# Kernel tuning notes

Measured on AMD Instinct MI355X. Metric: run time of the kernel, lower is better.

The kernel has to match this reference:

```python
import jax, jax.numpy as jnp
import numpy as np

N_NODES = 50000
N_EDGES = 600000
F_IN = 128
H_DIM = 256
N_CLASSES = 16
N_GRAPHS = 64


def _sage_conv(x, edge_index, W_l, W_r, b, num_nodes):
    # PyG SAGEConv (aggr='mean', root_weight=True):
    #   out = lin_l(mean_{j in N(i)} x_j) + lin_r(x_i)
    src, dst = edge_index[0], edge_index[1]
    msg_sum = jax.ops.segment_sum(x[src], dst, num_segments=num_nodes)      # [N, F]
    cnt = jax.ops.segment_sum(jnp.ones((edge_index.shape[1],), x.dtype), dst,
                              num_segments=num_nodes)                        # [N]
    mean = msg_sum / jnp.maximum(cnt, 1.0)[:, None]
    return mean @ W_l + x @ W_r + b


def _global_mean_pool(x, batch, num_graphs):
    s = jax.ops.segment_sum(x, batch, num_segments=num_graphs)               # [G, C]
    c = jax.ops.segment_sum(jnp.ones((x.shape[0],), x.dtype), batch,
                            num_segments=num_graphs)                         # [G]
    return s / jnp.maximum(c, 1.0)[:, None]


def setup_inputs() -> dict:
    key = jax.random.key(0)
    ks = jax.random.split(key, 9)
    x = jax.random.normal(ks[0], (N_NODES, F_IN), dtype=jnp.float32)
    edge_index = jax.random.randint(ks[1], (2, N_EDGES), 0, N_NODES)
    batch = jnp.sort(jax.random.randint(ks[2], (N_NODES,), 0, N_GRAPHS))
    # SAGEConv params (glorot-ish scale)
    def w(k, fi, fo):
        return jax.random.normal(k, (fi, fo), dtype=jnp.float32) / np.sqrt(fi)
    return {
        "x": x,
        "edge_index": edge_index,
        "batch": batch,
        "W1_l": w(ks[3], F_IN, H_DIM),
        "W1_r": w(ks[4], F_IN, H_DIM),
        "b1": jnp.zeros((H_DIM,), jnp.float32),
        "W2_l": w(ks[5], H_DIM, N_CLASSES),
        "W2_r": w(ks[6], H_DIM, N_CLASSES),
        "b2": jnp.zeros((N_CLASSES,), jnp.float32),
    }


def reference(x, edge_index, batch, W1_l, W1_r, b1, W2_l, W2_r, b2):
    n = x.shape[0]
    h = _sage_conv(x, edge_index, W1_l, W1_r, b1, n)
    h = jax.nn.relu(h)
    h = _sage_conv(h, edge_index, W2_l, W2_r, b2, n)
    h = jax.nn.relu(h)
    g = _global_mean_pool(h, batch, N_GRAPHS)
    return jax.nn.log_softmax(g, axis=1)
```

## Files before the change

### kernel.cpp

```cpp
#include <hip/hip_runtime.h>

#define N_NODES   50000
#define N_EDGES   600000
#define F_IN      128
#define H_DIM     256
#define N_CLASSES 16
#define N_GRAPHS  64
#define M_PAD     50048
#define MAX_DEG   64
#define ZERO_WORDS (50000 + 1024 + 64 + 1)

typedef unsigned short ushort_t;
typedef unsigned int   uint_t;
typedef __attribute__((ext_vector_type(8))) short bf16x8;
typedef __attribute__((ext_vector_type(4))) float f32x4;

__device__ inline ushort_t f2bf(float f) {
    union { float f; uint_t u; } v; v.f = f;
    uint_t r = v.u + 0x7FFF + ((v.u >> 16) & 1);
    return (ushort_t)(r >> 16);
}
__device__ inline float bf2f(uint_t u) {
    union { uint_t u; float f; } v; v.u = u << 16;
    return v.f;
}
__device__ inline void load_lds16(const void* g, void* l) {
    __builtin_amdgcn_global_load_lds(
        (const __attribute__((address_space(1))) void*)g,
        (__attribute__((address_space(3))) void*)l, 16, 0, 0);
}

__global__ __launch_bounds__(256) void prep_kernel(
    const float* __restrict__ x,
    const float* __restrict__ W1l, const float* __restrict__ W1r,
    const float* __restrict__ W2l, const float* __restrict__ W2r,
    uint_t* __restrict__ wszero, ushort_t* __restrict__ ha,
    ushort_t* __restrict__ Bt, ushort_t* __restrict__ Bt2) {
    const int t = blockIdx.x * blockDim.x + threadIdx.x;
    if (t < ZERO_WORDS) wszero[t] = 0u;
    if (t < 65536) {
        const int n = t >> 8, k = t & 255;
        const float v = (k < 128) ? W1l[k * H_DIM + n] : W1r[(k - 128) * H_DIM + n];
        Bt[n * 256 + k] = f2bf(v);
    } else if (t < 65536 + 8192) {
        const int t2 = t - 65536;
        const int c = t2 >> 8, k = t2 & 255;
        const float v = (c < 16) ? W2l[k * N_CLASSES + c] : W2r[k * N_CLASSES + (c - 16)];
        Bt2[c * 256 + k] = f2bf(v);
    }
    if (t >= N_NODES * 32) return;
    const int n = t >> 5, c = t & 31;
    const float4 v = *reinterpret_cast<const float4*>(x + (size_t)n * F_IN + c * 4);
    uint2 pk;
    pk.x = (uint_t)f2bf(v.x) | ((uint_t)f2bf(v.y) << 16);
    pk.y = (uint_t)f2bf(v.z) | ((uint_t)f2bf(v.w) << 16);
    *reinterpret_cast<uint2*>(ha + (size_t)n * 256 + 128 + c * 4) = pk;
}

__global__ void scatter_pad_kernel(const int* __restrict__ src,
                                   const int* __restrict__ dst,
                                   int* __restrict__ cnt,
                                   int* __restrict__ slots) {
    int e = blockIdx.x * blockDim.x + threadIdx.x;
    if (e >= N_EDGES) return;
    const int d = dst[e];
    const int pos = atomicAdd(&cnt[d], 1);
    if (pos < MAX_DEG) slots[d * MAX_DEG + pos] = src[e];
}

__global__ __launch_bounds__(256) void agg1_kernel(const int* __restrict__ cnt,
                                                   const int* __restrict__ slots,
                                                   ushort_t* __restrict__ ha,
                                                   float* __restrict__ invdeg) {
    const int n = blockIdx.x * 4 + (threadIdx.x >> 6);
    if (n >= N_NODES) return;
    const int lane = threadIdx.x & 63;
    const int slot = lane >> 3;
    const int c    = lane & 7;
    const int deg  = min(cnt[n], MAX_DEG);
    const int* srow = slots + n * MAX_DEG;
    float a[16];
#pragma unroll
    for (int i = 0; i < 16; ++i) a[i] = 0.f;
    for (int e = slot; e < deg; e += 16) {
        const int s0 = srow[e];
        const ushort_t* r0 = ha + (size_t)s0 * 256 + 128;
        const uint4 v00 = *reinterpret_cast<const uint4*>(r0 + c * 8);
        const uint4 v01 = *reinterpret_cast<const uint4*>(r0 + 64 + c * 8);
        const int e1 = e + 8;
        uint4 v10, v11;
        if (e1 < deg) {
            const int s1 = srow[e1];
            const ushort_t* r1 = ha + (size_t)s1 * 256 + 128;
            v10 = *reinterpret_cast<const uint4*>(r1 + c * 8);
            v11 = *reinterpret_cast<const uint4*>(r1 + 64 + c * 8);
        }
        a[0] += bf2f(v00.x & 0xFFFFu); a[1] += bf2f(v00.x >> 16);
        a[2] += bf2f(v00.y & 0xFFFFu); a[3] += bf2f(v00.y >> 16);
        a[4] += bf2f(v00.z & 0xFFFFu); a[5] += bf2f(v00.z >> 16);
        a[6] += bf2f(v00.w & 0xFFFFu); a[7] += bf2f(v00.w >> 16);
        a[8]  += bf2f(v01.x & 0xFFFFu); a[9]  += bf2f(v01.x >> 16);
        a[10] += bf2f(v01.y & 0xFFFFu); a[11] += bf2f(v01.y >> 16);
        a[12] += bf2f(v01.z & 0xFFFFu); a[13] += bf2f(v01.z >> 16);
        a[14] += bf2f(v01.w & 0xFFFFu); a[15] += bf2f(v01.w >> 16);
        if (e1 < deg) {
            a[0] += bf2f(v10.x & 0xFFFFu); a[1] += bf2f(v10.x >> 16);
            a[2] += bf2f(v10.y & 0xFFFFu); a[3] += bf2f(v10.y >> 16);
            a[4] += bf2f(v10.z & 0xFFFFu); a[5] += bf2f(v10.z >> 16);
            a[6] += bf2f(v10.w & 0xFFFFu); a[7] += bf2f(v10.w >> 16);
            a[8]  += bf2f(v11.x & 0xFFFFu); a[9]  += bf2f(v11.x >> 16);
            a[10] += bf2f(v11.y & 0xFFFFu); a[11] += bf2f(v11.y >> 16);
            a[12] += bf2f(v11.z & 0xFFFFu); a[13] += bf2f(v11.z >> 16);
            a[14] += bf2f(v11.w & 0xFFFFu); a[15] += bf2f(v11.w >> 16);
        }
    }
#pragma unroll
    for (int i = 0; i < 16; ++i) {
        a[i] += __shfl_xor(a[i], 8);
        a[i] += __shfl_xor(a[i], 16);
        a[i] += __shfl_xor(a[i], 32);
    }
    const float iv = 1.0f / fmaxf((float)deg, 1.0f);
    if (slot == 0) {
        uint4 pk0, pk1;
        pk0.x = (uint_t)f2bf(a[0] * iv) | ((uint_t)f2bf(a[1] * iv) << 16);
        pk0.y = (uint_t)f2bf(a[2] * iv) | ((uint_t)f2bf(a[3] * iv) << 16);
        pk0.z = (uint_t)f2bf(a[4] * iv) | ((uint_t)f2bf(a[5] * iv) << 16);
        pk0.w = (uint_t)f2bf(a[6] * iv) | ((uint_t)f2bf(a[7] * iv) << 16);
        pk1.x = (uint_t)f2bf(a[8]  * iv) | ((uint_t)f2bf(a[9]  * iv) << 16);
        pk1.y = (uint_t)f2bf(a[10] * iv) | ((uint_t)f2bf(a[11] * iv) << 16);
        pk1.z = (uint_t)f2bf(a[12] * iv) | ((uint_t)f2bf(a[13] * iv) << 16);
        pk1.w = (uint_t)f2bf(a[14] * iv) | ((uint_t)f2bf(a[15] * iv) << 16);
        ushort_t* orow = ha + (size_t)n * 256;
        *reinterpret_cast<uint4*>(orow + c * 8) = pk0;
        *reinterpret_cast<uint4*>(orow + 64 + c * 8) = pk1;
        if (c == 0) invdeg[n] = iv;
    }
}

__global__ __launch_bounds__(256) void gemm1_fused_kernel(
    const ushort_t* __restrict__ ha, const ushort_t* __restrict__ Bt,
    const ushort_t* __restrict__ Bt2, const float* __restrict__ b1,
    float* __restrict__ p, float* __restrict__ r) {
    __shared__ ushort_t sA[64 * 256];
    __shared__ ushort_t sB[32 * 256];
    const int tid  = threadIdx.x;
    const int mblk = blockIdx.x;

    const char* gA = (const char*)ha + (size_t)mblk * 32768;
    const char* gB = (const char*)Bt;
#pragma unroll
    for (int i = 0; i < 8; ++i) {
        const int d = (i * 256 + tid) * 16;
        const int s = d ^ (((d >> 9) & 7) << 4);
        load_lds16(gA + s, (char*)sA + (d & ~1023));
    }
#pragma unroll
    for (int i = 0; i < 4; ++i) {
        const int d = (i * 256 + tid) * 16;
        const int s = d ^ (((d >> 9) & 7) << 4);
        load_lds16(gB + s, (char*)sB + (d & ~1023));
    }
    __syncthreads();

    const int w    = tid >> 6;
    const int lane = tid & 63;
    const int lr   = lane & 15;
    const int hi   = lane >> 4;
    const int m0   = w * 16;

    bf16x8 afr[8];
    {
        const int row = m0 + lr;
        const int sw = (row & 7) << 4;
#pragma unroll
        for (int ks = 0; ks < 8; ++ks)
            afr[ks] = *reinterpret_cast<const bf16x8*>(
                (const char*)sA + ((row * 512 + ks * 64 + hi * 16) ^ sw));
    }

    f32x4 acc[16];
#pragma unroll
    for (int t = 0; t < 16; ++t) acc[t] = (f32x4){0.f, 0.f, 0.f, 0.f};

#pragma unroll
    for (int ph = 0; ph < 8; ++ph) {
#pragma unroll
        for (int fnl = 0; fnl < 2; ++fnl) {
            const int rn = fnl * 16 + lr;
            const int sw = (rn & 7) << 4;
#pragma unroll
            for (int ks = 0; ks < 8; ++ks) {
                const bf16x8 bfr = *reinterpret_cast<const bf16x8*>(
                    (const char*)sB + ((rn * 512 + ks * 64 + hi * 16) ^ sw));
                acc[ph * 2 + fnl] = __builtin_amdgcn_mfma_f32_16x16x32_bf16(
                    afr[ks], bfr, acc[ph * 2 + fnl], 0, 0, 0);
            }
        }
        __syncthreads();
        if (ph < 7) {
#pragma unroll
            for (int i = 0; i < 4; ++i) {
                const int d = (i * 256 + tid) * 16;
                const int s = d ^ (((d >> 9) & 7) << 4);
                load_lds16(gB + (ph + 1) * 16384 + s, (char*)sB + (d & ~1023));
            }
            __syncthreads();
        }
    }

#pragma unroll
    for (int t = 0; t < 16; ++t) {
        const int colG = t * 16 + lr;
        const float bias = b1[colG];
#pragma unroll
        for (int i = 0; i < 4; ++i) {
            const int row = m0 + hi * 4 + i;
            const float h = fmaxf(acc[t][i] + bias, 0.f);
            const int ad = (row * 512 + colG * 2) ^ ((row & 7) << 4);
            *reinterpret_cast<ushort_t*>((char*)sA + ad) = f2bf(h);
        }
    }
    __syncthreads();

    const char* bt2b = (const char*)Bt2;
    const int nr = m0 + lr;
    const int swn = (nr & 7) << 4;
    f32x4 acc2[2] = {(f32x4){0.f, 0.f, 0.f, 0.f}, (f32x4){0.f, 0.f, 0.f, 0.f}};
#pragma unroll
    for (int fc = 0; fc < 2; ++fc) {
#pragma unroll
        for (int k2 = 0; k2 < 8; ++k2) {
            const bf16x8 a2 = *reinterpret_cast<const bf16x8*>(
                bt2b + (fc * 16 + lr) * 512 + k2 * 64 + hi * 16);
            const bf16x8 b2 = *reinterpret_cast<const bf16x8*>(
                (const char*)sA + ((nr * 512 + k2 * 64 + hi * 16) ^ swn));
            acc2[fc] = __builtin_amdgcn_mfma_f32_16x16x32_bf16(a2, b2, acc2[fc], 0, 0, 0);
        }
    }

    const int node = mblk * 64 + nr;
    if (node < N_NODES) {
#pragma unroll
        for (int i = 0; i < 4; ++i) {
            p[(size_t)node * N_CLASSES + hi * 4 + i] = acc2[0][i];
            r[(size_t)node * N_CLASSES + hi * 4 + i] = acc2[1][i];
        }
    }
}

__global__ __launch_bounds__(256) void agg2_kernel(const float* __restrict__ p,
                                                   const int* __restrict__ cnt,
                                                   const int* __restrict__ slots,
                                                   float* __restrict__ psum) {
    const int n = blockIdx.x * 4 + (threadIdx.x >> 6);
    if (n >= N_NODES) return;
    const int lane = threadIdx.x & 63;
    const int slot = lane >> 2;
    const int c    = lane & 3;
    const int deg  = min(cnt[n], MAX_DEG);
    const int* srow = slots + n * MAX_DEG;
    float4 acc = {0.f, 0.f, 0.f, 0.f};
    for (int e = slot; e < deg; e += 16) {
        const int s = srow[e];
        const float4 v = *reinterpret_cast<const float4*>(p + (size_t)s * N_CLASSES + c * 4);
        acc.x += v.x; acc.y += v.y; acc.z += v.z; acc.w += v.w;
    }
#pragma unroll
    for (int o = 4; o < 64; o <<= 1) {
        acc.x += __shfl_xor(acc.x, o);
        acc.y += __shfl_xor(acc.y, o);
        acc.z += __shfl_xor(acc.z, o);
        acc.w += __shfl_xor(acc.w, o);
    }
    if (slot == 0)
        *reinterpret_cast<float4*>(psum + (size_t)n * N_CLASSES + c * 4) = acc;
}

__global__ __launch_bounds__(256) void pool_lsm_kernel(
    const float* __restrict__ psum, const float* __restrict__ r,
    const float* __restrict__ invdeg, const float* __restrict__ b2,
    const int* __restrict__ batch,
    float* __restrict__ gsum, float* __restrict__ gcnt,
    int* __restrict__ done, float* __restrict__ out, int nblocks) {
    __shared__ float lgsum[N_GRAPHS * N_CLASSES];
    __shared__ float lgcnt[N_GRAPHS];
    __shared__ int gminmax[2];
    __shared__ int last;
    const int t = threadIdx.x;
    const int base = blockIdx.x * 64;
#pragma unroll
    for (int k = 0; k < 4; ++k) lgsum[t + 256 * k] = 0.f;
    if (t < N_GRAPHS) lgcnt[t] = 0.f;
    if (t == 0) {
        gminmax[0] = batch[base];
        int lastn = base + 63; if (lastn >= N_NODES) lastn = N_NODES - 1;
        gminmax[1] = batch[lastn];
    }
    __syncthreads();

    const int j = t & 15;
    const float bj = b2[j];
#pragma unroll
    for (int k = 0; k < 4; ++k) {
        const int i = base + (t >> 4) + 16 * k;
        if (i < N_NODES) {
            float h = psum[(size_t)i * N_CLASSES + j] * invdeg[i]
                      + r[(size_t)i * N_CLASSES + j] + bj;
            h = fmaxf(h, 0.f);
            const int g = batch[i];
            atomicAdd(&lgsum[g * N_CLASSES + j], h);
            if (j == 0) atomicAdd(&lgcnt[g], 1.0f);
        }
    }
    __syncthreads();

    const int gmin = gminmax[0], gmax = gminmax[1];
    for (int gg = gmin + (t >> 4); gg <= gmax; gg += 16) {
        const float v = lgsum[gg * N_CLASSES + j];
        if (v != 0.f) atomicAdd(&gsum[gg * N_CLASSES + j], v);
    }
    if (t < N_GRAPHS) {
        const int gg = gmin + t;
        if (gg <= gmax) {
            const float c = lgcnt[gg];
            if (c != 0.f) atomicAdd(&gcnt[gg], c);
        }
    }
    __syncthreads();

    if (t == 0) {
        __threadfence();
        const int old = __hip_atomic_fetch_add(done, 1, __ATOMIC_ACQ_REL,
                                               __HIP_MEMORY_SCOPE_AGENT);
        last = (old == nblocks - 1) ? 1 : 0;
    }
    __syncthreads();

    if (last && t < N_GRAPHS) {
        const int g = t;
        const float cg = __hip_atomic_load(&gcnt[g], __ATOMIC_RELAXED,
                                           __HIP_MEMORY_SCOPE_AGENT);
        const float iv = 1.0f / fmaxf(cg, 1.0f);
        float v[N_CLASSES];
        float m = -1e30f;
#pragma unroll
        for (int jj = 0; jj < N_CLASSES; ++jj) {
            v[jj] = __hip_atomic_load(&gsum[g * N_CLASSES + jj], __ATOMIC_RELAXED,
                                      __HIP_MEMORY_SCOPE_AGENT) * iv;
            m = fmaxf(m, v[jj]);
        }
        float s = 0.f;
#pragma unroll
        for (int jj = 0; jj < N_CLASSES; ++jj) s += expf(v[jj] - m);
        const float lse = logf(s);
#pragma unroll
        for (int jj = 0; jj < N_CLASSES; ++jj)
            out[g * N_CLASSES + jj] = v[jj] - m - lse;
    }
}

extern "C" void kernel_launch(void* const* d_in, const int* in_sizes, int n_in,
                              void* d_out, int out_size, void* d_ws, size_t ws_size,
                              hipStream_t stream) {
    const float* x    = (const float*)d_in[0];
    const int*   ei   = (const int*)d_in[1];
    const int*   batch= (const int*)d_in[2];
    const float* W1l  = (const float*)d_in[3];
    const float* W1r  = (const float*)d_in[4];
    const float* b1   = (const float*)d_in[5];
    const float* W2l  = (const float*)d_in[6];
    const float* W2r  = (const float*)d_in[7];
    const float* b2   = (const float*)d_in[8];
    float* out = (float*)d_out;

    const int* src = ei;
    const int* dst = ei + N_EDGES;

    float* ws     = (float*)d_ws;
    int*   cnt    = (int*)ws;
    float* gsum   = ws + 50000;
    float* gcnt   = gsum + 1024;
    int*   done   = (int*)(gcnt + 64);
    float* invdeg = (float*)(done + 1);
    int*   slots  = (int*)(invdeg + 50000);
    ushort_t* Bt  = (ushort_t*)(slots + 3200000 + 3);
    ushort_t* Bt2 = Bt + 65536;
    ushort_t* ha  = Bt2 + 8192;
    float* p      = (float*)(ha + (size_t)M_PAD * 256);
    float* r      = p + 800000;
    float* psum   = (float*)ha;

    const int PB = 782;
    prep_kernel<<<(N_NODES * 32 + 255) / 256, 256, 0, stream>>>(
        x, W1l, W1r, W2l, W2r, (uint_t*)ws, ha, Bt, Bt2);
    scatter_pad_kernel<<<(N_EDGES + 255) / 256, 256, 0, stream>>>(src, dst, cnt, slots);
    agg1_kernel<<<(N_NODES + 3) / 4, 256, 0, stream>>>(cnt, slots, ha, invdeg);
    gemm1_fused_kernel<<<M_PAD / 64, 256, 0, stream>>>(ha, Bt, Bt2, b1, p, r);
    agg2_kernel<<<(N_NODES + 3) / 4, 256, 0, stream>>>(p, cnt, slots, psum);
    pool_lsm_kernel<<<PB, 256, 0, stream>>>(psum, r, invdeg, b2, batch,
                                            gsum, gcnt, done, out, PB);
}
```

Measured before the change: 150.6 us.

## Double-buffer weight tiles in GEMM1 and store layer-2 messages as bf16

The GEMM1 kernel now double-buffers the B-matrix tile in LDS, issuing the next phase's load before the current MFMA loop and dropping one barrier per phase. The layer-2 projected messages p are written as bf16 instead of fp32 with vectorized stores, and agg2 gathers 16-byte bf16 rows with 32 edge slots per wave. This halves the bytes moved in the random-gather aggregation and overlaps weight loads with compute. The cost is extra LDS per block and bf16 rounding of the layer-2 messages before summation.

```diff
diff --git a/kernel.cpp b/kernel.cpp
--- a/kernel.cpp
+++ b/kernel.cpp
@@ -141,9 +141,9 @@
 __global__ __launch_bounds__(256) void gemm1_fused_kernel(
     const ushort_t* __restrict__ ha, const ushort_t* __restrict__ Bt,
     const ushort_t* __restrict__ Bt2, const float* __restrict__ b1,
-    float* __restrict__ p, float* __restrict__ r) {
+    ushort_t* __restrict__ pb, float* __restrict__ r) {
     __shared__ ushort_t sA[64 * 256];
-    __shared__ ushort_t sB[32 * 256];
+    __shared__ ushort_t sB[2][32 * 256];
     const int tid  = threadIdx.x;
     const int mblk = blockIdx.x;
 
@@ -159,7 +159,7 @@
     for (int i = 0; i < 4; ++i) {
         const int d = (i * 256 + tid) * 16;
         const int s = d ^ (((d >> 9) & 7) << 4);
-        load_lds16(gB + s, (char*)sB + (d & ~1023));
+        load_lds16(gB + s, (char*)sB[0] + (d & ~1023));
     }
     __syncthreads();
 
@@ -185,6 +185,16 @@
 
 #pragma unroll
     for (int ph = 0; ph < 8; ++ph) {
+        if (ph < 7) {
+#pragma unroll
+            for (int i = 0; i < 4; ++i) {
+                const int d = (i * 256 + tid) * 16;
+                const int s = d ^ (((d >> 9) & 7) << 4);
+                load_lds16(gB + (ph + 1) * 16384 + s,
+                           (char*)sB[(ph + 1) & 1] + (d & ~1023));
+            }
+        }
+        const char* sbp = (const char*)sB[ph & 1];
 #pragma unroll
         for (int fnl = 0; fnl < 2; ++fnl) {
             const int rn = fnl * 16 + lr;
@@ -192,21 +202,12 @@
 #pragma unroll
             for (int ks = 0; ks < 8; ++ks) {
                 const bf16x8 bfr = *reinterpret_cast<const bf16x8*>(
-                    (const char*)sB + ((rn * 512 + ks * 64 + hi * 16) ^ sw));
+                    sbp + ((rn * 512 + ks * 64 + hi * 16) ^ sw));
                 acc[ph * 2 + fnl] = __builtin_amdgcn_mfma_f32_16x16x32_bf16(
                     afr[ks], bfr, acc[ph * 2 + fnl], 0, 0, 0);
             }
         }
         __syncthreads();
-        if (ph < 7) {
-#pragma unroll
-            for (int i = 0; i < 4; ++i) {
-                const int d = (i * 256 + tid) * 16;
-                const int s = d ^ (((d >> 9) & 7) << 4);
-                load_lds16(gB + (ph + 1) * 16384 + s, (char*)sB + (d & ~1023));
-            }
-            __syncthreads();
-        }
     }
 
 #pragma unroll
@@ -241,40 +242,50 @@
 
     const int node = mblk * 64 + nr;
     if (node < N_NODES) {
-#pragma unroll
-        for (int i = 0; i < 4; ++i) {
-            p[(size_t)node * N_CLASSES + hi * 4 + i] = acc2[0][i];
-            r[(size_t)node * N_CLASSES + hi * 4 + i] = acc2[1][i];
-        }
-    }
-}
-
-__global__ __launch_bounds__(256) void agg2_kernel(const float* __restrict__ p,
+        uint2 pp;
+        pp.x = (uint_t)f2bf(acc2[0][0]) | ((uint_t)f2bf(acc2[0][1]) << 16);
+        pp.y = (uint_t)f2bf(acc2[0][2]) | ((uint_t)f2bf(acc2[0][3]) << 16);
+        *reinterpret_cast<uint2*>(pb + (size_t)node * N_CLASSES + hi * 4) = pp;
+        float4 rv = {acc2[1][0], acc2[1][1], acc2[1][2], acc2[1][3]};
+        *reinterpret_cast<float4*>(r + (size_t)node * N_CLASSES + hi * 4) = rv;
+    }
+}
+
+__global__ __launch_bounds__(256) void agg2_kernel(const ushort_t* __restrict__ pb,
                                                    const int* __restrict__ cnt,
                                                    const int* __restrict__ slots,
                                                    float* __restrict__ psum) {
     const int n = blockIdx.x * 4 + (threadIdx.x >> 6);
     if (n >= N_NODES) return;
     const int lane = threadIdx.x & 63;
-    const int slot = lane >> 2;
-    const int c    = lane & 3;
+    const int slot = lane >> 1;
+    const int c    = lane & 1;
     const int deg  = min(cnt[n], MAX_DEG);
     const int* srow = slots + n * MAX_DEG;
-    float4 acc = {0.f, 0.f, 0.f, 0.f};
-    for (int e = slot; e < deg; e += 16) {
+    float a[8];
+#pragma unroll
+    for (int i = 0; i < 8; ++i) a[i] = 0.f;
+    for (int e = slot; e < deg; e += 32) {
         const int s = srow[e];
-        const float4 v = *reinterpret_cast<const float4*>(p + (size_t)s * N_CLASSES + c * 4);
-        acc.x += v.x; acc.y += v.y; acc.z += v.z; acc.w += v.w;
-    }
-#pragma unroll
-    for (int o = 4; o < 64; o <<= 1) {
-        acc.x += __shfl_xor(acc.x, o);
-        acc.y += __shfl_xor(acc.y, o);
-        acc.z += __shfl_xor(acc.z, o);
-        acc.w += __shfl_xor(acc.w, o);
-    }
-    if (slot == 0)
-        *reinterpret_cast<float4*>(psum + (size_t)n * N_CLASSES + c * 4) = acc;
+        const uint4 v = *reinterpret_cast<const uint4*>(pb + (size_t)s * N_CLASSES + c * 8);
+        a[0] += bf2f(v.x & 0xFFFFu); a[1] += bf2f(v.x >> 16);
+        a[2] += bf2f(v.y & 0xFFFFu); a[3] += bf2f(v.y >> 16);
+        a[4] += bf2f(v.z & 0xFFFFu); a[5] += bf2f(v.z >> 16);
+        a[6] += bf2f(v.w & 0xFFFFu); a[7] += bf2f(v.w >> 16);
+    }
+#pragma unroll
+    for (int i = 0; i < 8; ++i) {
+        a[i] += __shfl_xor(a[i], 2);
+        a[i] += __shfl_xor(a[i], 4);
+        a[i] += __shfl_xor(a[i], 8);
+        a[i] += __shfl_xor(a[i], 16);
+        a[i] += __shfl_xor(a[i], 32);
+    }
+    if (slot == 0) {
+        float* orow = psum + (size_t)n * N_CLASSES + c * 8;
+        *reinterpret_cast<float4*>(orow)     = (float4){a[0], a[1], a[2], a[3]};
+        *reinterpret_cast<float4*>(orow + 4) = (float4){a[4], a[5], a[6], a[7]};
+    }
 }
 
 __global__ __launch_bounds__(256) void pool_lsm_kernel(
@@ -387,8 +398,8 @@
     ushort_t* Bt  = (ushort_t*)(slots + 3200000 + 3);
     ushort_t* Bt2 = Bt + 65536;
     ushort_t* ha  = Bt2 + 8192;
-    float* p      = (float*)(ha + (size_t)M_PAD * 256);
-    float* r      = p + 800000;
+    ushort_t* pb  = ha + (size_t)M_PAD * 256;
+    float* r      = (float*)(pb + (size_t)M_PAD * 16);
     float* psum   = (float*)ha;
 
     const int PB = 782;
@@ -396,8 +407,8 @@
         x, W1l, W1r, W2l, W2r, (uint_t*)ws, ha, Bt, Bt2);
     scatter_pad_kernel<<<(N_EDGES + 255) / 256, 256, 0, stream>>>(src, dst, cnt, slots);
     agg1_kernel<<<(N_NODES + 3) / 4, 256, 0, stream>>>(cnt, slots, ha, invdeg);
-    gemm1_fused_kernel<<<M_PAD / 64, 256, 0, stream>>>(ha, Bt, Bt2, b1, p, r);
-    agg2_kernel<<<(N_NODES + 3) / 4, 256, 0, stream>>>(p, cnt, slots, psum);
+    gemm1_fused_kernel<<<M_PAD / 64, 256, 0, stream>>>(ha, Bt, Bt2, b1, pb, r);
+    agg2_kernel<<<(N_NODES + 3) / 4, 256, 0, stream>>>(pb, cnt, slots, psum);
     pool_lsm_kernel<<<PB, 256, 0, stream>>>(psum, r, invdeg, b2, batch,
                                             gsum, gcnt, done, out, PB);
 }
```

Result: slower. 159.5 us (+5.9%).

## Fuse layer-2 aggregation into pooling kernel and store projected features as bf16

Applied to the files above, without the earlier changes.

Removes the separate agg2 kernel and performs the neighbor gather-sum of layer-2 projected features inside the pooling kernel, which now handles 16 nodes per block. The projected p values are written as bf16 to halve the bytes gathered per edge, and the r/p stores become vectorized. This saves one launch and the psum write/read round trip, but gives up some accuracy in the layer-2 messages and means more blocks do shared-memory atomics and global flushes.

```diff
diff --git a/kernel.cpp b/kernel.cpp
--- a/kernel.cpp
+++ b/kernel.cpp
@@ -9,6 +9,7 @@
 #define M_PAD     50048
 #define MAX_DEG   64
 #define ZERO_WORDS (50000 + 1024 + 64 + 1)
+#define POOL_BLOCKS (M_PAD / 16)
 
 typedef unsigned short ushort_t;
 typedef unsigned int   uint_t;
@@ -141,7 +142,7 @@
 __global__ __launch_bounds__(256) void gemm1_fused_kernel(
     const ushort_t* __restrict__ ha, const ushort_t* __restrict__ Bt,
     const ushort_t* __restrict__ Bt2, const float* __restrict__ b1,
-    float* __restrict__ p, float* __restrict__ r) {
+    ushort_t* __restrict__ pb, float* __restrict__ r) {
     __shared__ ushort_t sA[64 * 256];
     __shared__ ushort_t sB[32 * 256];
     const int tid  = threadIdx.x;
@@ -241,46 +242,20 @@
 
     const int node = mblk * 64 + nr;
     if (node < N_NODES) {
-#pragma unroll
-        for (int i = 0; i < 4; ++i) {
-            p[(size_t)node * N_CLASSES + hi * 4 + i] = acc2[0][i];
-            r[(size_t)node * N_CLASSES + hi * 4 + i] = acc2[1][i];
-        }
-    }
-}
-
-__global__ __launch_bounds__(256) void agg2_kernel(const float* __restrict__ p,
-                                                   const int* __restrict__ cnt,
-                                                   const int* __restrict__ slots,
-                                                   float* __restrict__ psum) {
-    const int n = blockIdx.x * 4 + (threadIdx.x >> 6);
-    if (n >= N_NODES) return;
-    const int lane = threadIdx.x & 63;
-    const int slot = lane >> 2;
-    const int c    = lane & 3;
-    const int deg  = min(cnt[n], MAX_DEG);
-    const int* srow = slots + n * MAX_DEG;
-    float4 acc = {0.f, 0.f, 0.f, 0.f};
-    for (int e = slot; e < deg; e += 16) {
-        const int s = srow[e];
-        const float4 v = *reinterpret_cast<const float4*>(p + (size_t)s * N_CLASSES + c * 4);
-        acc.x += v.x; acc.y += v.y; acc.z += v.z; acc.w += v.w;
-    }
-#pragma unroll
-    for (int o = 4; o < 64; o <<= 1) {
-        acc.x += __shfl_xor(acc.x, o);
-        acc.y += __shfl_xor(acc.y, o);
-        acc.z += __shfl_xor(acc.z, o);
-        acc.w += __shfl_xor(acc.w, o);
-    }
-    if (slot == 0)
-        *reinterpret_cast<float4*>(psum + (size_t)n * N_CLASSES + c * 4) = acc;
+        uint2 pp;
+        pp.x = (uint_t)f2bf(acc2[0][0]) | ((uint_t)f2bf(acc2[0][1]) << 16);
+        pp.y = (uint_t)f2bf(acc2[0][2]) | ((uint_t)f2bf(acc2[0][3]) << 16);
+        *reinterpret_cast<uint2*>(pb + (size_t)node * N_CLASSES + hi * 4) = pp;
+        float4 rv = {acc2[1][0], acc2[1][1], acc2[1][2], acc2[1][3]};
+        *reinterpret_cast<float4*>(r + (size_t)node * N_CLASSES + hi * 4) = rv;
+    }
 }
 
 __global__ __launch_bounds__(256) void pool_lsm_kernel(
-    const float* __restrict__ psum, const float* __restrict__ r,
+    const ushort_t* __restrict__ pb, const float* __restrict__ r,
     const float* __restrict__ invdeg, const float* __restrict__ b2,
     const int* __restrict__ batch,
+    const int* __restrict__ cnt, const int* __restrict__ slots,
     float* __restrict__ gsum, float* __restrict__ gcnt,
     int* __restrict__ done, float* __restrict__ out, int nblocks) {
     __shared__ float lgsum[N_GRAPHS * N_CLASSES];
@@ -288,34 +263,62 @@
     __shared__ int gminmax[2];
     __shared__ int last;
     const int t = threadIdx.x;
-    const int base = blockIdx.x * 64;
+    const int base = blockIdx.x * 16;
 #pragma unroll
     for (int k = 0; k < 4; ++k) lgsum[t + 256 * k] = 0.f;
     if (t < N_GRAPHS) lgcnt[t] = 0.f;
     if (t == 0) {
-        gminmax[0] = batch[base];
-        int lastn = base + 63; if (lastn >= N_NODES) lastn = N_NODES - 1;
-        gminmax[1] = batch[lastn];
-    }
-    __syncthreads();
-
+        gminmax[0] = batch[min(base, N_NODES - 1)];
+        gminmax[1] = batch[min(base + 15, N_NODES - 1)];
+    }
+    __syncthreads();
+
+    const int w    = t >> 6;
+    const int lane = t & 63;
+    const int slot = lane >> 2;
+    const int c    = lane & 3;
+#pragma unroll
+    for (int i = 0; i < 4; ++i) {
+        const int n = base + w * 4 + i;
+        if (n >= N_NODES) break;
+        const int deg = min(cnt[n], MAX_DEG);
+        const int* srow = slots + n * MAX_DEG;
+        float a0 = 0.f, a1 = 0.f, a2 = 0.f, a3 = 0.f;
+        for (int e = slot; e < deg; e += 16) {
+            const int s = srow[e];
+            const uint2 v = *reinterpret_cast<const uint2*>(
+                pb + (size_t)s * N_CLASSES + c * 4);
+            a0 += bf2f(v.x & 0xFFFFu); a1 += bf2f(v.x >> 16);
+            a2 += bf2f(v.y & 0xFFFFu); a3 += bf2f(v.y >> 16);
+        }
+#pragma unroll
+        for (int o = 4; o < 64; o <<= 1) {
+            a0 += __shfl_xor(a0, o);
+            a1 += __shfl_xor(a1, o);
+            a2 += __shfl_xor(a2, o);
+            a3 += __shfl_xor(a3, o);
+        }
+        if (slot == 0) {
+            const float iv = invdeg[n];
+            const float4 rv = *reinterpret_cast<const float4*>(
+                r + (size_t)n * N_CLASSES + c * 4);
+            const float4 bv = *reinterpret_cast<const float4*>(b2 + c * 4);
+            const float h0 = fmaxf(a0 * iv + rv.x + bv.x, 0.f);
+            const float h1 = fmaxf(a1 * iv + rv.y + bv.y, 0.f);
+            const float h2 = fmaxf(a2 * iv + rv.z + bv.z, 0.f);
+            const float h3 = fmaxf(a3 * iv + rv.w + bv.w, 0.f);
+            const int g = batch[n];
+            atomicAdd(&lgsum[g * N_CLASSES + c * 4 + 0], h0);
+            atomicAdd(&lgsum[g * N_CLASSES + c * 4 + 1], h1);
+            atomicAdd(&lgsum[g * N_CLASSES + c * 4 + 2], h2);
+            atomicAdd(&lgsum[g * N_CLASSES + c * 4 + 3], h3);
+            if (c == 0) atomicAdd(&lgcnt[g], 1.0f);
+        }
+    }
+    __syncthreads();
+
+    const int gmin = gminmax[0], gmax = gminmax[1];
     const int j = t & 15;
-    const float bj = b2[j];
-#pragma unroll
-    for (int k = 0; k < 4; ++k) {
-        const int i = base + (t >> 4) + 16 * k;
-        if (i < N_NODES) {
-            float h = psum[(size_t)i * N_CLASSES + j] * invdeg[i]
-                      + r[(size_t)i * N_CLASSES + j] + bj;
-            h = fmaxf(h, 0.f);
-            const int g = batch[i];
-            atomicAdd(&lgsum[g * N_CLASSES + j], h);
-            if (j == 0) atomicAdd(&lgcnt[g], 1.0f);
-        }
-    }
-    __syncthreads();
-
-    const int gmin = gminmax[0], gmax = gminmax[1];
     for (int gg = gmin + (t >> 4); gg <= gmax; gg += 16) {
         const float v = lgsum[gg * N_CLASSES + j];
         if (v != 0.f) atomicAdd(&gsum[gg * N_CLASSES + j], v);
@@ -323,8 +326,8 @@
     if (t < N_GRAPHS) {
         const int gg = gmin + t;
         if (gg <= gmax) {
-            const float c = lgcnt[gg];
-            if (c != 0.f) atomicAdd(&gcnt[gg], c);
+            const float cv = lgcnt[gg];
+            if (cv != 0.f) atomicAdd(&gcnt[gg], cv);
         }
     }
     __syncthreads();
@@ -387,17 +390,15 @@
     ushort_t* Bt  = (ushort_t*)(slots + 3200000 + 3);
     ushort_t* Bt2 = Bt + 65536;
     ushort_t* ha  = Bt2 + 8192;
-    float* p      = (float*)(ha + (size_t)M_PAD * 256);
-    float* r      = p + 800000;
-    float* psum   = (float*)ha;
-
-    const int PB = 782;
+    ushort_t* pb  = ha + (size_t)M_PAD * 256;
+    float* r      = (float*)(pb + (size_t)M_PAD * 16);
+
     prep_kernel<<<(N_NODES * 32 + 255) / 256, 256, 0, stream>>>(
         x, W1l, W1r, W2l, W2r, (uint_t*)ws, ha, Bt, Bt2);
     scatter_pad_kernel<<<(N_EDGES + 255) / 256, 256, 0, stream>>>(src, dst, cnt, slots);
     agg1_kernel<<<(N_NODES + 3) / 4, 256, 0, stream>>>(cnt, slots, ha, invdeg);
-    gemm1_fused_kernel<<<M_PAD / 64, 256, 0, stream>>>(ha, Bt, Bt2, b1, p, r);
-    agg2_kernel<<<(N_NODES + 3) / 4, 256, 0, stream>>>(p, cnt, slots, psum);
-    pool_lsm_kernel<<<PB, 256, 0, stream>>>(psum, r, invdeg, b2, batch,
-                                            gsum, gcnt, done, out, PB);
-}
+    gemm1_fused_kernel<<<M_PAD / 64, 256, 0, stream>>>(ha, Bt, Bt2, b1, pb, r);
+    pool_lsm_kernel<<<POOL_BLOCKS, 256, 0, stream>>>(pb, r, invdeg, b2, batch,
+                                                     cnt, slots, gsum, gcnt,
+                                                     done, out, POOL_BLOCKS);
+}
```

Result: slower. 235.6 us (+56.4%).
